# Kernel tuning notes

Measured on AMD Instinct MI355X. Metric: run time of the kernel, lower is better.

Reference implementation:

```python
import jax, jax.numpy as jnp
import numpy as np
import math

GROUPS = 32
EPS = 1e-5
NUM_HEADS = 8


def group_norm(x, gamma, beta):
    # x: [B, C, T]
    B, C, T = x.shape
    xg = x.reshape(B, GROUPS, C // GROUPS, T)
    mean = xg.mean(axis=(2, 3), keepdims=True)
    var = xg.var(axis=(2, 3), keepdims=True)
    xn = (xg - mean) * jax.lax.rsqrt(var + EPS)
    return xn.reshape(B, C, T) * gamma[None, :, None] + beta[None, :, None]


def qkv_attention(qkv, num_heads):
    # qkv: [B, 3C, T]
    B, C3, T = qkv.shape
    split = C3 // (3 * num_heads)  # head dim
    q, k, v = jnp.split(qkv, 3, axis=1)
    scale = 1.0 / math.sqrt(math.sqrt(split))
    q = (q * scale).reshape(B * num_heads, split, T)
    k = (k * scale).reshape(B * num_heads, split, T)
    v = v.reshape(B * num_heads, split, T)
    w = jnp.einsum('bct,bcs->bts', q, k)
    w = jax.nn.softmax(w.astype(jnp.float32), axis=-1).astype(w.dtype)
    out = jnp.einsum('bts,bcs->bct', w, v)
    return out.reshape(B, -1, T)


def setup_inputs() -> dict:
    key = jax.random.key(0)
    ks = jax.random.split(key, 6)
    B, C, H, W = 16, 512, 32, 32
    x = jax.random.normal(ks[0], (B, C, H, W), dtype=jnp.float32)
    gamma = jnp.ones((C,), jnp.float32)
    beta = jnp.zeros((C,), jnp.float32)
    w_qkv = jax.random.normal(ks[1], (3 * C, C), jnp.float32) * (1.0 / math.sqrt(C))
    b_qkv = jax.random.normal(ks[2], (3 * C,), jnp.float32) * 0.01
    # proj is zero-initialized in the module; use small random weights so the
    # full op chain (proj + residual) is numerically exercised.
    w_proj = jax.random.normal(ks[3], (C, C), jnp.float32) * (1.0 / math.sqrt(C))
    b_proj = jax.random.normal(ks[4], (C,), jnp.float32) * 0.01
    return {"x": x, "gamma": gamma, "beta": beta, "w_qkv": w_qkv,
            "b_qkv": b_qkv, "w_proj": w_proj, "b_proj": b_proj}


def reference(x, gamma, beta, w_qkv, b_qkv, w_proj, b_proj):
    b, c = x.shape[0], x.shape[1]
    spatial = x.shape[2:]
    xf = x.reshape(b, c, -1)                     # [B, C, T]
    xn = group_norm(xf, gamma, beta)
    qkv = jnp.einsum('oc,bct->bot', w_qkv, xn) + b_qkv[None, :, None]
    h = qkv_attention(qkv, NUM_HEADS)
    h = jnp.einsum('oc,bct->bot', w_proj, h) + b_proj[None, :, None]
    # NOTE: residual uses the normalized x (x is reassigned before norm in torch code)
    return (xn + h).reshape(b, c, *spatial)
```

## Files before the change

### kernel.cpp

```cpp
#include <hip/hip_runtime.h>

typedef __attribute__((ext_vector_type(8))) short s16x8;
typedef __attribute__((ext_vector_type(8))) unsigned short u16x8;
typedef __attribute__((ext_vector_type(4))) float f32x4;
typedef __attribute__((ext_vector_type(16))) float f32x16;

#define DEV static __device__ __forceinline__

DEV unsigned short f2bf(float f){
  union { float f; unsigned u; } v; v.f = f;
  unsigned u = v.u;
  return (unsigned short)((u + 0x7FFFu + ((u >> 16) & 1u)) >> 16);
}

DEV unsigned cvt_pk(float lo, float hi){
  unsigned r;
  asm("v_cvt_pk_bf16_f32 %0, %1, %2" : "=v"(r) : "v"(lo), "v"(hi));
  return r;
}

DEV void gload16(const void* g, void* l){
  __builtin_amdgcn_global_load_lds((const __attribute__((address_space(1))) void*)g,
                                   (__attribute__((address_space(3))) void*)l, 16, 0, 0);
}

DEV unsigned usel(bool c, unsigned a, unsigned b){ return c ? a : b; }

__global__ __launch_bounds__(256) void k_cvt(const float* __restrict__ src,
                                             unsigned short* __restrict__ dst, int n4){
  int i = blockIdx.x * 256 + threadIdx.x;
  if (i >= n4) return;
  float4 v = ((const float4*)src)[i];
  unsigned long long p = (unsigned long long)f2bf(v.x)
                       | ((unsigned long long)f2bf(v.y) << 16)
                       | ((unsigned long long)f2bf(v.z) << 32)
                       | ((unsigned long long)f2bf(v.w) << 48);
  *(unsigned long long*)(dst + (size_t)i * 4) = p;
}

__global__ __launch_bounds__(256) void k_gn(const float* __restrict__ x,
    const float* __restrict__ gamma, const float* __restrict__ beta,
    float* __restrict__ stats, unsigned short* __restrict__ xt){
  __shared__ unsigned short lt[1024 * 16];
  __shared__ float red[8];
  __shared__ float sh_ms[2];
  const int b = blockIdx.x >> 5, g = blockIdx.x & 31;
  const int tid = threadIdx.x;
  const float* base = x + ((size_t)(b * 512 + g * 16)) * 1024;

  float4 vv[16];
  float s = 0.f, ss = 0.f;
  #pragma unroll
  for (int i = 0; i < 16; ++i){
    vv[i] = *(const float4*)(base + i * 1024 + tid * 4);
    s  += vv[i].x + vv[i].y + vv[i].z + vv[i].w;
    ss += vv[i].x * vv[i].x + vv[i].y * vv[i].y + vv[i].z * vv[i].z + vv[i].w * vv[i].w;
  }
  #pragma unroll
  for (int d = 1; d < 64; d <<= 1){ s += __shfl_xor(s, d); ss += __shfl_xor(ss, d); }
  if ((tid & 63) == 0){ red[tid >> 6] = s; red[4 + (tid >> 6)] = ss; }
  __syncthreads();
  if (tid == 0){
    float ts  = red[0] + red[1] + red[2] + red[3];
    float tss = red[4] + red[5] + red[6] + red[7];
    float mean = ts * (1.f / 16384.f);
    float var  = tss * (1.f / 16384.f) - mean * mean;
    float rstd = rsqrtf(var + 1e-5f);
    sh_ms[0] = mean; sh_ms[1] = rstd;
    stats[(size_t)blockIdx.x * 2] = mean;
    stats[(size_t)blockIdx.x * 2 + 1] = rstd;
  }
  __syncthreads();
  const float mean = sh_ms[0], rstd = sh_ms[1];

  unsigned short vals[4][16];
  #pragma unroll
  for (int i = 0; i < 16; ++i){
    float gsc = gamma[g * 16 + i] * rstd;
    float bof = beta[g * 16 + i] - mean * gsc;
    vals[0][i] = f2bf(vv[i].x * gsc + bof);
    vals[1][i] = f2bf(vv[i].y * gsc + bof);
    vals[2][i] = f2bf(vv[i].z * gsc + bof);
    vals[3][i] = f2bf(vv[i].w * gsc + bof);
  }
  #pragma unroll
  for (int k2 = 0; k2 < 4; ++k2){
    u16x8 lo, hi;
    #pragma unroll
    for (int e = 0; e < 8; ++e){ lo[e] = vals[k2][e]; hi[e] = vals[k2][8 + e]; }
    int t = tid * 4 + k2;
    *(u16x8*)&lt[t * 16]     = lo;
    *(u16x8*)&lt[t * 16 + 8] = hi;
  }
  __syncthreads();
  unsigned short* dst = xt + ((size_t)b * 1024) * 512 + g * 16;
  #pragma unroll
  for (int j = 0; j < 8; ++j){
    int idx = j * 256 + tid;
    int t = idx >> 1, half = idx & 1;
    u16x8 v = *(const u16x8*)&lt[t * 16 + half * 8];
    *(u16x8*)(dst + (size_t)t * 512 + half * 8) = v;
  }
}

DEV void gemm_mainloop(const unsigned short* __restrict__ pA,
                       const unsigned short* __restrict__ pB,
                       unsigned short* As, unsigned short* Bs,
                       f32x4 (&acc)[4][4], int tid){
  const int lane = tid & 63, wv = tid >> 6;
  const int wr = wv >> 1, wc = wv & 1;
  const int ro = lane & 15;
  for (int k0 = 0; k0 < 512; k0 += 64){
    #pragma unroll
    for (int it = 0; it < 4; ++it){
      int chunk = it * 256 + tid;
      int r = chunk >> 3, sb = chunk & 7;
      size_t goff = (size_t)r * 512 + k0 + ((sb ^ (r & 7)) << 3);
      gload16(pA + goff, As + (size_t)(it * 256 + wv * 64) * 8);
      gload16(pB + goff, Bs + (size_t)(it * 256 + wv * 64) * 8);
    }
    __syncthreads();
    #pragma unroll
    for (int kk = 0; kk < 2; ++kk){
      s16x8 a[4], bb[4];
      int ko = kk * 64 + ((lane >> 4) << 4);
      #pragma unroll
      for (int i2 = 0; i2 < 4; ++i2){
        int ra = wr * 64 + i2 * 16 + ro;
        a[i2]  = *(const s16x8*)((const char*)As + ra * 128 + (ko ^ ((ra & 7) << 4)));
        int rb = wc * 64 + i2 * 16 + ro;
        bb[i2] = *(const s16x8*)((const char*)Bs + rb * 128 + (ko ^ ((rb & 7) << 4)));
      }
      __builtin_amdgcn_s_setprio(1);
      #pragma unroll
      for (int i2 = 0; i2 < 4; ++i2)
        #pragma unroll
        for (int j2 = 0; j2 < 4; ++j2)
          acc[i2][j2] = __builtin_amdgcn_mfma_f32_16x16x32_bf16(a[i2], bb[j2], acc[i2][j2], 0, 0, 0);
      __builtin_amdgcn_s_setprio(0);
    }
    __syncthreads();
  }
}

__global__ __launch_bounds__(256) void k_qkv(const unsigned short* __restrict__ W,
    const unsigned short* __restrict__ Xt, const float* __restrict__ bias,
    unsigned short* __restrict__ qkt, unsigned short* __restrict__ vbuf){
  __shared__ unsigned short As[128 * 64], Bs[128 * 64];
  const int bid = blockIdx.x;
  const int nt = bid & 7; const int tmp = bid >> 3;
  const int mt = tmp % 12, b = tmp / 12;
  const int tid = threadIdx.x;
  const unsigned short* Wt = W + (size_t)mt * 128 * 512;
  const unsigned short* Xb = Xt + ((size_t)(b * 1024) + nt * 128) * 512;
  f32x4 acc[4][4];
  #pragma unroll
  for (int i = 0; i < 4; ++i)
    #pragma unroll
    for (int j = 0; j < 4; ++j) acc[i][j] = f32x4{0.f, 0.f, 0.f, 0.f};
  const bool isv = (mt >= 8);
  if (isv) gemm_mainloop(Wt, Xb, As, Bs, acc, tid);
  else     gemm_mainloop(Xb, Wt, As, Bs, acc, tid);
  const int lane = tid & 63, wv = tid >> 6, wr = wv >> 1, wc = wv & 1;
  const int col = lane & 15, rq = (lane >> 4) << 2;
  if (isv){
    #pragma unroll
    for (int i = 0; i < 4; ++i){
      #pragma unroll
      for (int jj = 0; jj < 4; ++jj){
        int og = mt * 128 + wr * 64 + i * 16 + rq + jj;
        float bv = bias[og];
        unsigned short* drow = vbuf + ((size_t)(b * 512) + (og - 1024)) * 1024 + nt * 128 + wc * 64;
        #pragma unroll
        for (int j = 0; j < 4; ++j)
          drow[j * 16 + col] = f2bf(acc[i][j][jj] + bv);
      }
    }
  } else {
    #pragma unroll
    for (int i = 0; i < 4; ++i){
      #pragma unroll
      for (int jj = 0; jj < 4; ++jj){
        int tg = nt * 128 + wr * 64 + i * 16 + rq + jj;
        unsigned short* drow = qkt + ((size_t)(b * 1024) + tg) * 1024 + mt * 128 + wc * 64;
        #pragma unroll
        for (int j = 0; j < 4; ++j){
          int og = mt * 128 + wc * 64 + j * 16 + col;
          drow[j * 16 + col] = f2bf(acc[i][j][jj] + bias[og]);
        }
      }
    }
  }
}

__global__ __launch_bounds__(256, 4) void k_attn(const unsigned short* __restrict__ qkt,
    const unsigned short* __restrict__ vbuf, unsigned short* __restrict__ ht){
  __shared__ __align__(16) unsigned short smem[16384];

  const int bid = blockIdx.x;
  const int xcd = bid & 7, slot = bid >> 3;
  const int qt = slot & 7;
  const int b = slot >> 3, h = xcd;
  const int tid = threadIdx.x, lane = tid & 63, wv = tid >> 6;
  const int l31 = lane & 31, hi = lane >> 5;
  const int wq0 = qt * 128 + wv * 32;
  const float CSC = 0.125f * 1.44269504f;
  const float M0 = 8.f;

  s16x8 qf[4];
  {
    const unsigned short* qrow = qkt + ((size_t)(b * 1024) + wq0 + l31) * 1024 + h * 64 + hi * 8;
    #pragma unroll
    for (int kk = 0; kk < 4; ++kk)
      qf[kk] = *(const s16x8*)(qrow + kk * 16);
  }

  f32x16 o_acc[2];
  #pragma unroll
  for (int mi = 0; mi < 2; ++mi)
    #pragma unroll
    for (int e = 0; e < 16; ++e) o_acc[mi][e] = 0.f;
  float l_run = 0.f;

  const unsigned short* Kg = qkt + (size_t)(b * 1024) * 1024 + 512 + h * 64;
  const unsigned short* Vg = vbuf + ((size_t)(b * 512) + h * 64) * 1024;

  #define STAGE(s0, bsel) do {                                                          \
    unsigned short* Kd = smem + (bsel) * 8192;                                          \
    unsigned short* Vd = Kd + 4096;                                                     \
    _Pragma("unroll")                                                                   \
    for (int it = 0; it < 2; ++it){                                                     \
      int chunk = it * 256 + tid;                                                       \
      int r = chunk >> 3, sb = chunk & 7;                                               \
      int so = (sb ^ (r & 7)) << 3;                                                     \
      gload16(Kg + (size_t)((s0) + r) * 1024 + so, Kd + (size_t)(it * 256 + wv * 64) * 8); \
      gload16(Vg + (size_t)r * 1024 + (s0) + so,   Vd + (size_t)(it * 256 + wv * 64) * 8); \
    }                                                                                   \
  } while (0)

  STAGE(0, 0);
  __syncthreads();
  int cur = 0;

  for (int t = 0; t < 16; ++t){
    if (t < 15) STAGE((t + 1) * 64, cur ^ 1);
    const unsigned short* Ks = smem + cur * 8192;
    const unsigned short* Vs = Ks + 4096;

    f32x16 sa[2];
    #pragma unroll
    for (int ni = 0; ni < 2; ++ni)
      #pragma unroll
      for (int e = 0; e < 16; ++e) sa[ni][e] = 0.f;
    #pragma unroll
    for (int kk = 0; kk < 4; ++kk){
      s16x8 kf[2];
      #pragma unroll
      for (int ni = 0; ni < 2; ++ni){
        int r = ni * 32 + l31;
        kf[ni] = *(const s16x8*)((const char*)Ks + r * 128 + ((kk * 32 + hi * 16) ^ ((r & 7) << 4)));
      }
      __builtin_amdgcn_s_setprio(1);
      sa[0] = __builtin_amdgcn_mfma_f32_32x32x16_bf16(kf[0], qf[kk], sa[0], 0, 0, 0);
      sa[1] = __builtin_amdgcn_mfma_f32_32x32x16_bf16(kf[1], qf[kk], sa[1], 0, 0, 0);
      __builtin_amdgcn_s_setprio(0);
    }

    float rsa = 0.f, rsb = 0.f;
    unsigned pk[2][4][2];
    #pragma unroll
    for (int ni = 0; ni < 2; ++ni)
      #pragma unroll
      for (int rr = 0; rr < 4; ++rr){
        float p0 = exp2f(fmaf(sa[ni][4 * rr + 0], CSC, -M0));
        float p1 = exp2f(fmaf(sa[ni][4 * rr + 1], CSC, -M0));
        float p2 = exp2f(fmaf(sa[ni][4 * rr + 2], CSC, -M0));
        float p3 = exp2f(fmaf(sa[ni][4 * rr + 3], CSC, -M0));
        rsa += p0 + p1;
        rsb += p2 + p3;
        pk[ni][rr][0] = cvt_pk(p0, p1);
        pk[ni][rr][1] = cvt_pk(p2, p3);
      }
    float rs = rsa + rsb;
    rs += __shfl_xor(rs, 32);
    l_run += rs;

    #pragma unroll
    for (int ks = 0; ks < 4; ++ks){
      int ni = ks >> 1, q2 = (ks & 1) * 2;
      unsigned L0 = pk[ni][q2][0],     L1 = pk[ni][q2][1];
      unsigned H0 = pk[ni][q2 + 1][0], H1 = pk[ni][q2 + 1][1];
      unsigned send0 = usel(hi, L0, H0);
      unsigned send1 = usel(hi, L1, H1);
      unsigned recv0 = __shfl_xor((int)send0, 32);
      unsigned recv1 = __shfl_xor((int)send1, 32);
      union { unsigned u[4]; s16x8 v; } pb;
      pb.u[0] = usel(hi, recv0, L0);
      pb.u[1] = usel(hi, recv1, L1);
      pb.u[2] = usel(hi, H0, recv0);
      pb.u[3] = usel(hi, H1, recv1);
      s16x8 vf[2];
      #pragma unroll
      for (int mi = 0; mi < 2; ++mi){
        int c = mi * 32 + l31;
        vf[mi] = *(const s16x8*)((const char*)Vs + c * 128 + ((ks * 32 + hi * 16) ^ ((c & 7) << 4)));
      }
      __builtin_amdgcn_s_setprio(1);
      o_acc[0] = __builtin_amdgcn_mfma_f32_32x32x16_bf16(vf[0], pb.v, o_acc[0], 0, 0, 0);
      o_acc[1] = __builtin_amdgcn_mfma_f32_32x32x16_bf16(vf[1], pb.v, o_acc[1], 0, 0, 0);
      __builtin_amdgcn_s_setprio(0);
    }

    asm volatile("s_waitcnt vmcnt(0)" ::: "memory");
    __builtin_amdgcn_sched_barrier(0);
    __syncthreads();
    cur ^= 1;
  }
  #undef STAGE

  float invl = 1.f / l_run;
  unsigned short* ow = smem + wv * 2048;
  int t = l31;
  #pragma unroll
  for (int mi = 0; mi < 2; ++mi)
    #pragma unroll
    for (int rr = 0; rr < 4; ++rr){
      int c0 = mi * 32 + 8 * rr + 4 * hi;
      unsigned d0 = cvt_pk(o_acc[mi][4 * rr + 0] * invl, o_acc[mi][4 * rr + 1] * invl);
      unsigned d1 = cvt_pk(o_acc[mi][4 * rr + 2] * invl, o_acc[mi][4 * rr + 3] * invl);
      unsigned* dst = (unsigned*)(ow + t * 64 + (c0 ^ ((t & 7) << 3)));
      dst[0] = d0; dst[1] = d1;
    }
  __syncthreads();
  unsigned short* hbase = ht + ((size_t)(b * 1024) + wq0) * 512 + h * 64;
  #pragma unroll
  for (int i = 0; i < 4; ++i){
    int id = i * 64 + lane;
    int tl = id >> 3, c8 = id & 7;
    u16x8 v = *(const u16x8*)(ow + tl * 64 + ((c8 ^ (tl & 7)) << 3));
    *(u16x8*)(hbase + (size_t)tl * 512 + c8 * 8) = v;
  }
}

__global__ __launch_bounds__(256) void k_proj(const unsigned short* __restrict__ Wp,
    const unsigned short* __restrict__ Ht, const float* __restrict__ bias,
    const float* __restrict__ x, const float* __restrict__ stats,
    const float* __restrict__ gamma, const float* __restrict__ beta,
    float* __restrict__ out){
  __shared__ unsigned short As[128 * 64], Bs[128 * 64];
  const int bid = blockIdx.x;
  const int nt = bid & 7, mt = (bid >> 3) & 3, b = bid >> 5;
  const int tid = threadIdx.x;
  f32x4 acc[4][4];
  #pragma unroll
  for (int i = 0; i < 4; ++i)
    #pragma unroll
    for (int j = 0; j < 4; ++j) acc[i][j] = f32x4{0.f, 0.f, 0.f, 0.f};
  gemm_mainloop(Wp + (size_t)mt * 128 * 512,
                Ht + ((size_t)(b * 1024) + nt * 128) * 512, As, Bs, acc, tid);
  const int lane = tid & 63, wv = tid >> 6, wr = wv >> 1, wc = wv & 1;
  const int col = lane & 15, rq = (lane >> 4) << 2;
  #pragma unroll
  for (int i = 0; i < 4; ++i){
    #pragma unroll
    for (int jj = 0; jj < 4; ++jj){
      int og = mt * 128 + wr * 64 + i * 16 + rq + jj;
      float mean = stats[(size_t)(b * 32 + (og >> 4)) * 2];
      float rstd = stats[(size_t)(b * 32 + (og >> 4)) * 2 + 1];
      float gsc = gamma[og] * rstd;
      float bof = beta[og] - mean * gsc + bias[og];
      const float* xrow = x  + ((size_t)(b * 512) + og) * 1024 + nt * 128 + wc * 64;
      float* orow      = out + ((size_t)(b * 512) + og) * 1024 + nt * 128 + wc * 64;
      #pragma unroll
      for (int j = 0; j < 4; ++j){
        float xv = xrow[j * 16 + col];
        orow[j * 16 + col] = acc[i][j][jj] + xv * gsc + bof;
      }
    }
  }
}

extern "C" void kernel_launch(void* const* d_in, const int* in_sizes, int n_in,
                              void* d_out, int out_size, void* d_ws, size_t ws_size,
                              hipStream_t stream) {
  (void)in_sizes; (void)n_in; (void)out_size; (void)ws_size;
  const float* x      = (const float*)d_in[0];
  const float* gamma  = (const float*)d_in[1];
  const float* beta   = (const float*)d_in[2];
  const float* w_qkv  = (const float*)d_in[3];
  const float* b_qkv  = (const float*)d_in[4];
  const float* w_proj = (const float*)d_in[5];
  const float* b_proj = (const float*)d_in[6];
  float* out = (float*)d_out;
  char* ws = (char*)d_ws;

  unsigned short* wq_bf = (unsigned short*)ws;
  unsigned short* wp_bf = (unsigned short*)(ws + 1572864);
  float*          stats = (float*)(ws + 2097152);
  unsigned short* Xt    = (unsigned short*)(ws + 2101248);
  unsigned short* qkt   = (unsigned short*)(ws + 18878464);
  unsigned short* vbuf  = (unsigned short*)(ws + 52432896);

  k_cvt<<<768, 256, 0, stream>>>(w_qkv, wq_bf, 196608);
  k_cvt<<<256, 256, 0, stream>>>(w_proj, wp_bf, 65536);
  k_gn<<<512, 256, 0, stream>>>(x, gamma, beta, stats, Xt);
  k_qkv<<<1536, 256, 0, stream>>>(wq_bf, Xt, b_qkv, qkt, vbuf);
  unsigned short* Ht = Xt;
  k_attn<<<1024, 256, 0, stream>>>(qkt, vbuf, Ht);
  k_proj<<<512, 256, 0, stream>>>(wp_bf, Ht, b_proj, x, stats, gamma, beta, out);
}
```

Baseline: 137.8 us.

## Software-pipeline attention loop so QK of next tile overlaps PV of previous

Restructures the flash-attention inner loop into a two-stage software pipeline: each iteration computes QK^T for the current key tile, then the PV product for the previous tile's probabilities, then softmax for the current tile. K uses a double buffer and V a triple-buffer ring in enlarged shared memory. The aim is to hide MFMA-to-exp dependency latency by interleaving independent matrix and transcendental work. The cost is more LDS per block (40KB instead of 32KB) and more live registers for two probability buffers, which may reduce occupancy.

```diff
diff --git a/kernel.cpp b/kernel.cpp
--- a/kernel.cpp
+++ b/kernel.cpp
@@ -195,7 +195,7 @@
 
 __global__ __launch_bounds__(256, 4) void k_attn(const unsigned short* __restrict__ qkt,
     const unsigned short* __restrict__ vbuf, unsigned short* __restrict__ ht){
-  __shared__ __align__(16) unsigned short smem[16384];
+  __shared__ __align__(16) unsigned short smem[20480];
 
   const int bid = blockIdx.x;
   const int xcd = bid & 7, slot = bid >> 3;
@@ -225,99 +225,133 @@
   const unsigned short* Kg = qkt + (size_t)(b * 1024) * 1024 + 512 + h * 64;
   const unsigned short* Vg = vbuf + ((size_t)(b * 512) + h * 64) * 1024;
 
-  #define STAGE(s0, bsel) do {                                                          \
-    unsigned short* Kd = smem + (bsel) * 8192;                                          \
-    unsigned short* Vd = Kd + 4096;                                                     \
-    _Pragma("unroll")                                                                   \
-    for (int it = 0; it < 2; ++it){                                                     \
-      int chunk = it * 256 + tid;                                                       \
-      int r = chunk >> 3, sb = chunk & 7;                                               \
-      int so = (sb ^ (r & 7)) << 3;                                                     \
+  #define STAGE_KV(s0, kdst_e, vdst_e) do {                                              \
+    unsigned short* Kd = smem + (kdst_e);                                                \
+    unsigned short* Vd = smem + (vdst_e);                                                \
+    _Pragma("unroll")                                                                    \
+    for (int it = 0; it < 2; ++it){                                                      \
+      int chunk = it * 256 + tid;                                                        \
+      int r = chunk >> 3, sb = chunk & 7;                                                \
+      int so = (sb ^ (r & 7)) << 3;                                                      \
       gload16(Kg + (size_t)((s0) + r) * 1024 + so, Kd + (size_t)(it * 256 + wv * 64) * 8); \
       gload16(Vg + (size_t)r * 1024 + (s0) + so,   Vd + (size_t)(it * 256 + wv * 64) * 8); \
-    }                                                                                   \
+    }                                                                                    \
   } while (0)
 
-  STAGE(0, 0);
-  __syncthreads();
-  int cur = 0;
-
-  for (int t = 0; t < 16; ++t){
-    if (t < 15) STAGE((t + 1) * 64, cur ^ 1);
-    const unsigned short* Ks = smem + cur * 8192;
-    const unsigned short* Vs = Ks + 4096;
-
-    f32x16 sa[2];
-    #pragma unroll
-    for (int ni = 0; ni < 2; ++ni)
-      #pragma unroll
-      for (int e = 0; e < 16; ++e) sa[ni][e] = 0.f;
-    #pragma unroll
-    for (int kk = 0; kk < 4; ++kk){
-      s16x8 kf[2];
-      #pragma unroll
-      for (int ni = 0; ni < 2; ++ni){
-        int r = ni * 32 + l31;
-        kf[ni] = *(const s16x8*)((const char*)Ks + r * 128 + ((kk * 32 + hi * 16) ^ ((r & 7) << 4)));
-      }
-      __builtin_amdgcn_s_setprio(1);
-      sa[0] = __builtin_amdgcn_mfma_f32_32x32x16_bf16(kf[0], qf[kk], sa[0], 0, 0, 0);
-      sa[1] = __builtin_amdgcn_mfma_f32_32x32x16_bf16(kf[1], qf[kk], sa[1], 0, 0, 0);
-      __builtin_amdgcn_s_setprio(0);
-    }
-
-    float rsa = 0.f, rsb = 0.f;
-    unsigned pk[2][4][2];
-    #pragma unroll
-    for (int ni = 0; ni < 2; ++ni)
-      #pragma unroll
-      for (int rr = 0; rr < 4; ++rr){
-        float p0 = exp2f(fmaf(sa[ni][4 * rr + 0], CSC, -M0));
-        float p1 = exp2f(fmaf(sa[ni][4 * rr + 1], CSC, -M0));
-        float p2 = exp2f(fmaf(sa[ni][4 * rr + 2], CSC, -M0));
-        float p3 = exp2f(fmaf(sa[ni][4 * rr + 3], CSC, -M0));
-        rsa += p0 + p1;
-        rsb += p2 + p3;
-        pk[ni][rr][0] = cvt_pk(p0, p1);
-        pk[ni][rr][1] = cvt_pk(p2, p3);
-      }
-    float rs = rsa + rsb;
-    rs += __shfl_xor(rs, 32);
-    l_run += rs;
-
-    #pragma unroll
-    for (int ks = 0; ks < 4; ++ks){
-      int ni = ks >> 1, q2 = (ks & 1) * 2;
-      unsigned L0 = pk[ni][q2][0],     L1 = pk[ni][q2][1];
-      unsigned H0 = pk[ni][q2 + 1][0], H1 = pk[ni][q2 + 1][1];
-      unsigned send0 = usel(hi, L0, H0);
-      unsigned send1 = usel(hi, L1, H1);
-      unsigned recv0 = __shfl_xor((int)send0, 32);
-      unsigned recv1 = __shfl_xor((int)send1, 32);
-      union { unsigned u[4]; s16x8 v; } pb;
-      pb.u[0] = usel(hi, recv0, L0);
-      pb.u[1] = usel(hi, recv1, L1);
-      pb.u[2] = usel(hi, H0, recv0);
-      pb.u[3] = usel(hi, H1, recv1);
-      s16x8 vf[2];
-      #pragma unroll
-      for (int mi = 0; mi < 2; ++mi){
-        int c = mi * 32 + l31;
-        vf[mi] = *(const s16x8*)((const char*)Vs + c * 128 + ((ks * 32 + hi * 16) ^ ((c & 7) << 4)));
-      }
-      __builtin_amdgcn_s_setprio(1);
-      o_acc[0] = __builtin_amdgcn_mfma_f32_32x32x16_bf16(vf[0], pb.v, o_acc[0], 0, 0, 0);
-      o_acc[1] = __builtin_amdgcn_mfma_f32_32x32x16_bf16(vf[1], pb.v, o_acc[1], 0, 0, 0);
-      __builtin_amdgcn_s_setprio(0);
-    }
-
-    asm volatile("s_waitcnt vmcnt(0)" ::: "memory");
-    __builtin_amdgcn_sched_barrier(0);
-    __syncthreads();
-    cur ^= 1;
-  }
-  #undef STAGE
-
+  #define QKBLOCK(KOFF) do {                                                             \
+    const unsigned short* Ks = smem + (KOFF);                                            \
+    _Pragma("unroll")                                                                    \
+    for (int ni = 0; ni < 2; ++ni)                                                       \
+      _Pragma("unroll")                                                                  \
+      for (int e = 0; e < 16; ++e) sa[ni][e] = 0.f;                                      \
+    _Pragma("unroll")                                                                    \
+    for (int kk = 0; kk < 4; ++kk){                                                      \
+      s16x8 kf[2];                                                                       \
+      _Pragma("unroll")                                                                  \
+      for (int ni = 0; ni < 2; ++ni){                                                    \
+        int r = ni * 32 + l31;                                                           \
+        kf[ni] = *(const s16x8*)((const char*)Ks + r * 128 + ((kk * 32 + hi * 16) ^ ((r & 7) << 4))); \
+      }                                                                                  \
+      __builtin_amdgcn_s_setprio(1);                                                     \
+      sa[0] = __builtin_amdgcn_mfma_f32_32x32x16_bf16(kf[0], qf[kk], sa[0], 0, 0, 0);    \
+      sa[1] = __builtin_amdgcn_mfma_f32_32x32x16_bf16(kf[1], qf[kk], sa[1], 0, 0, 0);    \
+      __builtin_amdgcn_s_setprio(0);                                                     \
+    }                                                                                    \
+  } while (0)
+
+  #define PVBLOCK(PK, VOFF) do {                                                         \
+    const unsigned short* Vs = smem + (VOFF);                                            \
+    _Pragma("unroll")                                                                    \
+    for (int ks = 0; ks < 4; ++ks){                                                      \
+      int ni = ks >> 1, q2 = (ks & 1) * 2;                                               \
+      unsigned L0 = PK[ni][q2][0],     L1 = PK[ni][q2][1];                               \
+      unsigned H0 = PK[ni][q2 + 1][0], H1 = PK[ni][q2 + 1][1];                           \
+      unsigned send0 = usel(hi, L0, H0);                                                 \
+      unsigned send1 = usel(hi, L1, H1);                                                 \
+      unsigned recv0 = __shfl_xor((int)send0, 32);                                       \
+      unsigned recv1 = __shfl_xor((int)send1, 32);                                       \
+      union { unsigned u[4]; s16x8 v; } pb;                                              \
+      pb.u[0] = usel(hi, recv0, L0);                                                     \
+      pb.u[1] = usel(hi, recv1, L1);                                                     \
+      pb.u[2] = usel(hi, H0, recv0);                                                     \
+      pb.u[3] = usel(hi, H1, recv1);                                                     \
+      s16x8 vf[2];                                                                       \
+      _Pragma("unroll")                                                                  \
+      for (int mi = 0; mi < 2; ++mi){                                                    \
+        int c = mi * 32 + l31;                                                           \
+        vf[mi] = *(const s16x8*)((const char*)Vs + c * 128 + ((ks * 32 + hi * 16) ^ ((c & 7) << 4))); \
+      }                                                                                  \
+      __builtin_amdgcn_s_setprio(1);                                                     \
+      o_acc[0] = __builtin_amdgcn_mfma_f32_32x32x16_bf16(vf[0], pb.v, o_acc[0], 0, 0, 0); \
+      o_acc[1] = __builtin_amdgcn_mfma_f32_32x32x16_bf16(vf[1], pb.v, o_acc[1], 0, 0, 0); \
+      __builtin_amdgcn_s_setprio(0);                                                     \
+    }                                                                                    \
+  } while (0)
+
+  #define SMBLOCK(PK) do {                                                               \
+    float rsa = 0.f, rsb = 0.f;                                                          \
+    _Pragma("unroll")                                                                    \
+    for (int ni = 0; ni < 2; ++ni)                                                       \
+      _Pragma("unroll")                                                                  \
+      for (int rr = 0; rr < 4; ++rr){                                                    \
+        float p0 = exp2f(fmaf(sa[ni][4 * rr + 0], CSC, -M0));                            \
+        float p1 = exp2f(fmaf(sa[ni][4 * rr + 1], CSC, -M0));                            \
+        float p2 = exp2f(fmaf(sa[ni][4 * rr + 2], CSC, -M0));                            \
+        float p3 = exp2f(fmaf(sa[ni][4 * rr + 3], CSC, -M0));                            \
+        rsa += p0 + p1;                                                                  \
+        rsb += p2 + p3;                                                                  \
+        PK[ni][rr][0] = cvt_pk(p0, p1);                                                  \
+        PK[ni][rr][1] = cvt_pk(p2, p3);                                                  \
+      }                                                                                  \
+    float rs = rsa + rsb;                                                                \
+    rs += __shfl_xor(rs, 32);                                                            \
+    l_run += rs;                                                                         \
+  } while (0)
+
+  #define DRAIN_BAR() do {                                                              \
+    asm volatile("s_waitcnt vmcnt(0)" ::: "memory");                                     \
+    __builtin_amdgcn_sched_barrier(0);                                                   \
+    __syncthreads();                                                                     \
+  } while (0)
+
+  STAGE_KV(0, 0, 8192);
+  __syncthreads();
+
+  unsigned pkA[2][4][2], pkB[2][4][2];
+  f32x16 sa[2];
+  int off_prev = 8192, off_cur = 8192, off_next = 12288;
+
+  for (int tp = 0; tp < 8; ++tp){
+    {
+      int t0 = 2 * tp;
+      STAGE_KV((t0 + 1) * 64, 4096, off_next);
+      QKBLOCK(0);
+      if (tp > 0) PVBLOCK(pkB, off_prev);
+      SMBLOCK(pkA);
+      off_prev = off_cur; off_cur = off_next;
+      off_next = (off_next == 16384) ? 8192 : off_next + 4096;
+      DRAIN_BAR();
+    }
+    {
+      int t1 = 2 * tp + 1;
+      if (tp < 7) STAGE_KV((t1 + 1) * 64, 0, off_next);
+      QKBLOCK(4096);
+      PVBLOCK(pkA, off_prev);
+      SMBLOCK(pkB);
+      off_prev = off_cur; off_cur = off_next;
+      off_next = (off_next == 16384) ? 8192 : off_next + 4096;
+      DRAIN_BAR();
+    }
+  }
+  PVBLOCK(pkB, off_prev);
+
+  #undef STAGE_KV
+  #undef QKBLOCK
+  #undef PVBLOCK
+  #undef SMBLOCK
+  #undef DRAIN_BAR
+
+  __syncthreads();
   float invl = 1.f / l_run;
   unsigned short* ow = smem + wv * 2048;
   int t = l31;
```

Measured after the change: 174.4 us. 1.27x slower.
